# Optimization experiments

Measured on AMD Instinct MI355X. Metric: run time of the kernel, lower is better.

Reference implementation:

```python
import jax, jax.numpy as jnp
import numpy as np

EPS = 1e-5
D = 4  # max_displacement


def _conv(x, w, b, stride, pad):
    # x: [B,C,H,W], w: [O,I,kh,kw]
    y = jax.lax.conv_general_dilated(x, w, (stride, stride), [(pad, pad), (pad, pad)],
                                     dimension_numbers=('NCHW', 'OIHW', 'NCHW'))
    return y + b[None, :, None, None]


def _bn(x, g, b, m, v):
    # eval-mode batchnorm with running stats
    scale = (g * jax.lax.rsqrt(v + EPS))[None, :, None, None]
    return (x - m[None, :, None, None]) * scale + b[None, :, None, None]


def _extract(x, w1, b1, g1, be1, m1, v1, w2, b2, g2, be2, m2, v2, w3, b3, g3, be3, m3, v3):
    x = jax.nn.relu(_bn(_conv(x, w1, b1, 2, 3), g1, be1, m1, v1))
    x = jax.nn.relu(_bn(_conv(x, w2, b2, 2, 1), g2, be2, m2, v2))
    x = jax.nn.relu(_bn(_conv(x, w3, b3, 2, 1), g3, be3, m3, v3))
    return x  # [B,256,H/8,W/8]


def _correlation(x1, x2):
    # shifted-window correlation, 81 shifts (structural loop, static slices)
    B, C, H, W = x1.shape
    x2p = jnp.pad(x2, ((0, 0), (0, 0), (D, D), (D, D)))
    maps = [jnp.sum(x1 * x2p[:, :, i:i + H, j:j + W], axis=1)
            for i in range(2 * D + 1) for j in range(2 * D + 1)]
    return jnp.stack(maps, axis=1)  # [B,81,H,W]


def _gmm(cloth_img, person_img, fe, fw1, fb1, fw2, fb2, fw3, fb3):
    cf = _extract(cloth_img, *fe)
    pf = _extract(person_img, *fe)
    corr = _correlation(cf, pf)
    x = jax.nn.relu(_conv(corr, fw1, fb1, 1, 1))
    x = jax.nn.relu(_conv(x, fw2, fb2, 1, 1))
    return _conv(x, fw3, fb3, 1, 1)  # [B,2,H/8,W/8]


def setup_inputs() -> dict:
    key = jax.random.key(0)
    ks = jax.random.split(key, 32)
    B, H, W = 8, 512, 512
    w = lambda k, shape, s=0.05: jax.random.normal(k, shape, jnp.float32) * s
    inp = {}
    inp['cloth_img'] = jax.random.normal(ks[0], (B, 3, H, W), jnp.float32)
    inp['person_img'] = jax.random.normal(ks[1], (B, 3, H, W), jnp.float32)
    inp['w1'] = w(ks[2], (64, 3, 7, 7)); inp['b1'] = w(ks[3], (64,))
    inp['g1'] = 1.0 + w(ks[4], (64,)); inp['be1'] = w(ks[5], (64,))
    inp['m1'] = w(ks[6], (64,)); inp['v1'] = jax.random.uniform(ks[7], (64,), jnp.float32, 0.5, 1.5)
    inp['w2'] = w(ks[8], (128, 64, 3, 3)); inp['b2'] = w(ks[9], (128,))
    inp['g2'] = 1.0 + w(ks[10], (128,)); inp['be2'] = w(ks[11], (128,))
    inp['m2'] = w(ks[12], (128,)); inp['v2'] = jax.random.uniform(ks[13], (128,), jnp.float32, 0.5, 1.5)
    inp['w3'] = w(ks[14], (256, 128, 3, 3)); inp['b3'] = w(ks[15], (256,))
    inp['g3'] = 1.0 + w(ks[16], (256,)); inp['be3'] = w(ks[17], (256,))
    inp['m3'] = w(ks[18], (256,)); inp['v3'] = jax.random.uniform(ks[19], (256,), jnp.float32, 0.5, 1.5)
    inp['fw1'] = w(ks[20], (128, 81, 3, 3)); inp['fb1'] = w(ks[21], (128,))
    inp['fw2'] = w(ks[22], (64, 128, 3, 3)); inp['fb2'] = w(ks[23], (64,))
    inp['fw3'] = w(ks[24], (2, 64, 3, 3)); inp['fb3'] = w(ks[25], (2,))
    return inp


def reference(cloth_img, person_img,
              w1, b1, g1, be1, m1, v1,
              w2, b2, g2, be2, m2, v2,
              w3, b3, g3, be3, m3, v3,
              fw1, fb1, fw2, fb2, fw3, fb3):
    fe = (w1, b1, g1, be1, m1, v1, w2, b2, g2, be2, m2, v2, w3, b3, g3, be3, m3, v3)
    return _gmm(cloth_img, person_img, fe, fw1, fb1, fw2, fb2, fw3, fb3)
```

## Files before the change

### kernel.cpp

```cpp
#include <hip/hip_runtime.h>

typedef __bf16 bf16x8_t __attribute__((ext_vector_type(8)));
typedef float f32x4 __attribute__((ext_vector_type(4)));
typedef unsigned short u16x8 __attribute__((ext_vector_type(8)));
typedef unsigned short u16x4 __attribute__((ext_vector_type(4)));

#define EPS 1e-5f

__device__ __forceinline__ unsigned short f2bf(float f) {
    unsigned u = __builtin_bit_cast(unsigned, f);
    u += 0x7fff + ((u >> 16) & 1);
    return (unsigned short)(u >> 16);
}

__device__ __forceinline__ void gload16(const unsigned short* g, unsigned short* l) {
    __builtin_amdgcn_global_load_lds(
        (const __attribute__((address_space(1))) unsigned int*)g,
        (__attribute__((address_space(3))) unsigned int*)l,
        16, 0, 0);
}

template <int N> __device__ __forceinline__ void s_waitcnt_vm() {
    if constexpr (N == 0)       asm volatile("s_waitcnt vmcnt(0)" ::: "memory");
    else if constexpr (N == 8)  asm volatile("s_waitcnt vmcnt(8)" ::: "memory");
    else if constexpr (N == 10) asm volatile("s_waitcnt vmcnt(10)" ::: "memory");
    else if constexpr (N == 12) asm volatile("s_waitcnt vmcnt(12)" ::: "memory");
    else static_assert(N == 0, "unsupported vmcnt");
}

__global__ void prep_affine_all(const float* __restrict__ b1, const float* __restrict__ g1,
                                const float* __restrict__ be1, const float* __restrict__ m1,
                                const float* __restrict__ v1,
                                const float* __restrict__ b2, const float* __restrict__ g2,
                                const float* __restrict__ be2, const float* __restrict__ m2,
                                const float* __restrict__ v2,
                                const float* __restrict__ b3, const float* __restrict__ g3,
                                const float* __restrict__ be3, const float* __restrict__ m3,
                                const float* __restrict__ v3,
                                const float* __restrict__ fb1, const float* __restrict__ fb2,
                                const float* __restrict__ fb3, float* __restrict__ aff) {
    int i = blockIdx.x * 256 + threadIdx.x;
    if (i < 64) {
        float s = g1[i] * rsqrtf(v1[i] + EPS);
        aff[i] = s; aff[64 + i] = (b1[i] - m1[i]) * s + be1[i];
    } else if (i < 192) {
        int c = i - 64; float s = g2[c] * rsqrtf(v2[c] + EPS);
        aff[128 + c] = s; aff[256 + c] = (b2[c] - m2[c]) * s + be2[c];
    } else if (i < 448) {
        int c = i - 192; float s = g3[c] * rsqrtf(v3[c] + EPS);
        aff[384 + c] = s; aff[640 + c] = (b3[c] - m3[c]) * s + be3[c];
    } else if (i < 576) {
        int c = i - 448; aff[896 + c] = 1.f; aff[1024 + c] = fb1[c];
    } else if (i < 640) {
        int c = i - 576; aff[1152 + c] = 1.f; aff[1216 + c] = fb2[c];
    } else if (i < 642) {
        int c = i - 640; aff[1280 + c] = 1.f; aff[1288 + c] = fb3[c];
    }
}

__device__ __forceinline__ void wconv3x3(const float* __restrict__ w, unsigned short* __restrict__ dst,
                                         int Cout, int Sp, int Kp, int CIN, int CINP, int idx) {
    if (idx >= Sp * Kp) return;
    int m = idx / Kp, k = idx - m * Kp;
    int tap = k / CINP, ic = k - tap * CINP;
    unsigned short v = 0;
    if (m < Cout && tap < 9 && ic < CIN) {
        int kh = tap / 3, kw = tap - kh * 3;
        v = f2bf(w[((m * CIN + ic) * 3 + kh) * 3 + kw]);
    }
    dst[idx] = v;
}

__global__ void conv_weights_all(const float* __restrict__ w1, const float* __restrict__ w2,
                                 const float* __restrict__ w3, const float* __restrict__ fw1,
                                 const float* __restrict__ fw2, const float* __restrict__ fw3,
                                 unsigned short* d1, unsigned short* d2, unsigned short* d3,
                                 unsigned short* d4, unsigned short* d5, unsigned short* d6) {
    int idx = blockIdx.x * 256 + threadIdx.x;
    switch (blockIdx.y) {
    case 0: {
        if (idx >= 64 * 256) return;
        int m = idx >> 8, k = idx & 255;
        int kh = k >> 5, r = k & 31, kw = r >> 2, ic = r & 3;
        unsigned short v = 0;
        if (kh < 7 && kw < 7 && ic < 3) v = f2bf(w1[((m * 3 + ic) * 7 + kh) * 7 + kw]);
        d1[idx] = v;
    } break;
    case 1: wconv3x3(w2, d2, 128, 128, 576, 64, 64, idx); break;
    case 2: wconv3x3(w3, d3, 256, 256, 1152, 128, 128, idx); break;
    case 3: wconv3x3(fw1, d4, 128, 128, 1152, 81, 128, idx); break;
    case 4: wconv3x3(fw2, d5, 64, 64, 1152, 128, 128, idx); break;
    case 5: wconv3x3(fw3, d6, 2, 64, 576, 64, 64, idx); break;
    }
}

__global__ void to_nhwc4(const float* __restrict__ cloth, const float* __restrict__ person,
                         unsigned short* __restrict__ dst) {
    int z = blockIdx.z;
    const float* src = (z < 8) ? cloth + (size_t)z * 786432
                               : person + (size_t)(z - 8) * 786432;
    int p = blockIdx.x * 256 + threadIdx.x;
    int row = p >> 9, col = p & 511;
    u16x4 o;
    o[0] = f2bf(src[p]);
    o[1] = f2bf(src[262144 + p]);
    o[2] = f2bf(src[524288 + p]);
    o[3] = 0;
    *(u16x4*)&dst[(size_t)z * 1073296 + ((size_t)(row + 3) * 518 + col + 3) * 4] = o;
}

__global__ void border_zero(unsigned short* __restrict__ buf, int Hp, int Wp, int C8,
                            int imgStrideElems, int nimg) {
    int idx = blockIdx.x * 256 + threadIdx.x;
    int nb = 2 * Wp + 2 * (Hp - 2);
    int per = nb * C8;
    if (idx >= per * nimg) return;
    int z = idx / per, q = idx - z * per;
    int p = q / C8, cc = q - p * C8;
    int row, col;
    if (p < Wp) { row = 0; col = p; }
    else if (p < 2 * Wp) { row = Hp - 1; col = p - Wp; }
    else { int e = p - 2 * Wp; row = 1 + (e >> 1); col = (e & 1) ? Wp - 1 : 0; }
    const u16x8 zv = {0, 0, 0, 0, 0, 0, 0, 0};
    *(u16x8*)&buf[(size_t)z * imgStrideElems + ((size_t)row * Wp + col) * (C8 * 8) + cc * 8] = zv;
}

template <int WR, int WS, int MODE, bool RELU, bool OUT_NCHW, int CIN, int NKT,
          int HIN, int WOS, int STRIDE, int OPAD>
__global__ __launch_bounds__(WR * WS * 64)
void gemm_conv(const unsigned short* __restrict__ X, const unsigned short* __restrict__ Wmk,
               const float* __restrict__ scale, const float* __restrict__ shift,
               void* __restrict__ Yv, int Cout, int xImgStride, int yImgStride) {
    constexpr int BR = WR * 64, BS = WS * 64, NT = WR * WS * 64;
    constexpr int SXC = BR * 8 / NT, SWC = BS * 8 / NT;
    constexpr int NLOAD = SXC + SWC;
    constexpr int KP = (MODE == 1) ? NKT * 64 : 256;
    constexpr int WP = HIN + ((MODE == 2) ? 6 : 2);
    constexpr int WOUT = 1 << WOS;
    constexpr int WOP = WOUT + 2 * OPAD;
    __shared__ __align__(16) unsigned short Xs[2][BR * 64];
    __shared__ __align__(16) unsigned short Ws[2][BS * 64];
    const int tid = threadIdx.x;
    const int lane = tid & 63, wid = tid >> 6;
    const int wr = wid % WR, wsx = wid / WR;
    int bx = blockIdx.x;
    { const int nx = gridDim.x; bx = (bx & 7) * (nx >> 3) + (bx >> 3); }
    const int r0 = bx * BR, s0 = blockIdx.y * BS;
    const int z = blockIdx.z;
    const int lr = lane & 15, lk = lane >> 4;
    const unsigned short* Ximg = X + (size_t)z * xImgStride;

    const unsigned short* xsrc[SXC];
    #pragma unroll
    for (int i = 0; i < SXC; ++i) {
        int c = i * NT + tid;
        int row = c >> 3, chs = (c & 7) ^ (row & 7);
        int r = r0 + row;
        int oh = r >> WOS, ow = r & (WOUT - 1);
        if (MODE == 1)
            xsrc[i] = Ximg + ((size_t)(oh * STRIDE) * WP + (size_t)(ow * STRIDE)) * CIN + chs * 8;
        else
            xsrc[i] = Ximg + ((size_t)(2 * oh + (chs >> 2)) * WP + 2 * ow + (chs & 3) * 2) * 4;
    }
    const unsigned short* wsrc[SWC];
    #pragma unroll
    for (int i = 0; i < SWC; ++i) {
        int c = i * NT + tid;
        int row = c >> 3, chs = (c & 7) ^ (row & 7);
        wsrc[i] = Wmk + (size_t)(s0 + row) * KP + chs * 8;
    }

    int arow[4], brow[4];
    #pragma unroll
    for (int mi = 0; mi < 4; ++mi) arow[mi] = (wr * 64 + mi * 16 + lr) * 64;
    #pragma unroll
    for (int si = 0; si < 4; ++si) brow[si] = (wsx * 64 + si * 16 + lr) * 64;

    const f32x4 fz = {0.f, 0.f, 0.f, 0.f};
    f32x4 acc[4][4];
    #pragma unroll
    for (int a = 0; a < 4; ++a)
        #pragma unroll
        for (int b = 0; b < 4; ++b) acc[a][b] = fz;

    auto stage = [&](int kt, int b) {
        size_t koff;
        if (MODE == 1) {
            const int tap = (kt * 64) / CIN;
            const int kh = tap / 3, kw = tap - (tap / 3) * 3;
            const int icb0 = (kt * 64) % CIN;
            koff = ((size_t)kh * WP + kw) * CIN + icb0;
        } else {
            koff = (size_t)kt * 2 * WP * 4;
        }
        #pragma unroll
        for (int i = 0; i < SXC; ++i) gload16(xsrc[i] + koff, &Xs[b][(i * NT + wid * 64) * 8]);
        #pragma unroll
        for (int i = 0; i < SWC; ++i) gload16(wsrc[i] + (size_t)kt * 64, &Ws[b][(i * NT + wid * 64) * 8]);
    };

    stage(0, 0);
    #pragma unroll
    for (int kt = 0; kt < NKT; ++kt) {
        const int cur = kt & 1;
        if (kt + 1 < NKT) {
            stage(kt + 1, cur ^ 1);
            s_waitcnt_vm<NLOAD>();
        } else {
            s_waitcnt_vm<0>();
        }
        __builtin_amdgcn_sched_barrier(0);
        __builtin_amdgcn_s_barrier();
        __builtin_amdgcn_sched_barrier(0);

        #pragma unroll
        for (int hf = 0; hf < 2; ++hf) {
            const int cA = (((hf * 4 + lk) ^ (lr & 7)) * 8);
            u16x8 af[4], bfr[4];
            #pragma unroll
            for (int mi = 0; mi < 4; ++mi) af[mi] = *(const u16x8*)&Xs[cur][arow[mi] + cA];
            #pragma unroll
            for (int si = 0; si < 4; ++si) bfr[si] = *(const u16x8*)&Ws[cur][brow[si] + cA];
            #pragma unroll
            for (int mi = 0; mi < 4; ++mi)
                #pragma unroll
                for (int si = 0; si < 4; ++si)
                    acc[mi][si] = __builtin_amdgcn_mfma_f32_16x16x32_bf16(
                        __builtin_bit_cast(bf16x8_t, af[mi]),
                        __builtin_bit_cast(bf16x8_t, bfr[si]), acc[mi][si], 0, 0, 0);
        }
        __builtin_amdgcn_sched_barrier(0);
        __builtin_amdgcn_s_barrier();
    }

    if (OUT_NCHW) {
        #pragma unroll
        for (int si = 0; si < 4; ++si) {
            int col = s0 + wsx * 64 + si * 16 + lr;
            bool cok = col < Cout;
            float sc = cok ? scale[col] : 0.f;
            float sh = cok ? shift[col] : 0.f;
            #pragma unroll
            for (int mi = 0; mi < 4; ++mi) {
                int rbase = r0 + wr * 64 + mi * 16 + lk * 4;
                #pragma unroll
                for (int j = 0; j < 4; ++j) {
                    float v = acc[mi][si][j] * sc + sh;
                    if (RELU) v = fmaxf(v, 0.f);
                    if (cok) ((float*)Yv)[(size_t)z * yImgStride + col * 4096 + rbase + j] = v;
                }
            }
        }
    } else {
        unsigned short* epi = (unsigned short*)Xs;
        #pragma unroll
        for (int si = 0; si < 4; ++si) {
            int col = wsx * 64 + si * 16 + lr;
            float sc = scale[s0 + col];
            float sh = shift[s0 + col];
            #pragma unroll
            for (int mi = 0; mi < 4; ++mi) {
                int rowl = wr * 64 + mi * 16 + lk * 4;
                #pragma unroll
                for (int j = 0; j < 4; ++j) {
                    float v = acc[mi][si][j] * sc + sh;
                    if (RELU) v = fmaxf(v, 0.f);
                    epi[(rowl + j) * BS + col] = f2bf(v);
                }
            }
        }
        __syncthreads();
        constexpr int NCH = BR * BS / 8 / NT;
        constexpr int CPR = BS / 8;
        #pragma unroll
        for (int i = 0; i < NCH; ++i) {
            int c = i * NT + tid;
            int row = c / CPR, colc = c - (c / CPR) * CPR;
            int r = r0 + row;
            int oh = r >> WOS, ow = r & (WOUT - 1);
            size_t off = ((size_t)(oh + OPAD) * WOP + ow + OPAD) * Cout + s0 + colc * 8;
            *(u16x8*)((unsigned short*)Yv + (size_t)z * yImgStride + off) =
                *(const u16x8*)&epi[row * BS + colc * 8];
        }
    }
}

__global__ __launch_bounds__(256)
void corr_mfma(const unsigned short* __restrict__ cf,
               const unsigned short* __restrict__ pf,
               unsigned short* __restrict__ out) {
    const int h = blockIdx.x;
    const int z = blockIdx.y;
    const int tid = threadIdx.x;
    const int lane = tid & 63, t = tid >> 6;
    const int lr = lane & 15, lk = lane >> 4;
    const unsigned short* cfi = cf + (size_t)z * 1048576;
    const unsigned short* pfi = pf + (size_t)z * 1048576;
    unsigned short* outp = out + (size_t)z * 557568;

    u16x8 a[8];
    {
        const unsigned short* ap = cfi + ((size_t)(h * 64 + t * 16 + lr)) * 256 + lk * 8;
        #pragma unroll
        for (int ks = 0; ks < 8; ++ks) a[ks] = *(const u16x8*)(ap + ks * 32);
    }

    const u16x8 zz = {0, 0, 0, 0, 0, 0, 0, 0};
    for (int di = -4; di <= 4; ++di) {
        const int h2 = h + di;
        const bool hok = (unsigned)h2 < 64u;
        #pragma unroll
        for (int ct = 0; ct < 2; ++ct) {
            const int wpg = t * 16 - 8 + ct * 16 + lr;
            u16x8 b[8];
            if (hok && (unsigned)wpg < 64u) {
                const unsigned short* bp = pfi + ((size_t)(h2 * 64 + wpg)) * 256 + lk * 8;
                #pragma unroll
                for (int ks = 0; ks < 8; ++ks) b[ks] = *(const u16x8*)(bp + ks * 32);
            } else {
                #pragma unroll
                for (int ks = 0; ks < 8; ++ks) b[ks] = zz;
            }
            f32x4 acc0 = {0.f, 0.f, 0.f, 0.f}, acc1 = {0.f, 0.f, 0.f, 0.f};
            #pragma unroll
            for (int ks = 0; ks < 8; ks += 2) {
                acc0 = __builtin_amdgcn_mfma_f32_16x16x32_bf16(
                    __builtin_bit_cast(bf16x8_t, a[ks]),
                    __builtin_bit_cast(bf16x8_t, b[ks]), acc0, 0, 0, 0);
                acc1 = __builtin_amdgcn_mfma_f32_16x16x32_bf16(
                    __builtin_bit_cast(bf16x8_t, a[ks + 1]),
                    __builtin_bit_cast(bf16x8_t, b[ks + 1]), acc1, 0, 0, 0);
            }
            const int wl = lk * 4;
            const int wpl = ct * 16 - 8 + lr;
            #pragma unroll
            for (int j = 0; j < 4; ++j) {
                int dj = wpl - (wl + j);
                if (dj >= -4 && dj <= 4) {
                    int s = (di + 4) * 9 + dj + 4;
                    int w = t * 16 + wl + j;
                    outp[((size_t)(h + 1) * 66 + w + 1) * 128 + s] =
                        f2bf(acc0[j] + acc1[j]);
                }
            }
        }
    }
}

extern "C" void kernel_launch(void* const* d_in, const int* in_sizes, int n_in,
                              void* d_out, int out_size, void* d_ws, size_t ws_size,
                              hipStream_t stream) {
    const float* cloth  = (const float*)d_in[0];
    const float* person = (const float*)d_in[1];
    const float* w1 = (const float*)d_in[2];  const float* b1 = (const float*)d_in[3];
    const float* g1 = (const float*)d_in[4];  const float* be1 = (const float*)d_in[5];
    const float* m1 = (const float*)d_in[6];  const float* v1 = (const float*)d_in[7];
    const float* w2 = (const float*)d_in[8];  const float* b2 = (const float*)d_in[9];
    const float* g2 = (const float*)d_in[10]; const float* be2 = (const float*)d_in[11];
    const float* m2 = (const float*)d_in[12]; const float* v2 = (const float*)d_in[13];
    const float* w3 = (const float*)d_in[14]; const float* b3 = (const float*)d_in[15];
    const float* g3 = (const float*)d_in[16]; const float* be3 = (const float*)d_in[17];
    const float* m3 = (const float*)d_in[18]; const float* v3 = (const float*)d_in[19];
    const float* fw1 = (const float*)d_in[20]; const float* fb1 = (const float*)d_in[21];
    const float* fw2 = (const float*)d_in[22]; const float* fb2 = (const float*)d_in[23];
    const float* fw3 = (const float*)d_in[24]; const float* fb3 = (const float*)d_in[25];

    char* ws = (char*)d_ws;
    auto U = [&](size_t off) { return (unsigned short*)(ws + off); };
    unsigned short* nhwc = U(0);
    unsigned short* t1   = U(34345472);
    unsigned short* cf   = U(34345472);
    unsigned short* t2   = U(170668544);
    unsigned short* w1mk  = U(239890944);
    unsigned short* w2mk  = U(239923712);
    unsigned short* w3mk  = U(240071168);
    unsigned short* fw1mk = U(240660992);
    unsigned short* fw2mk = U(240955904);
    unsigned short* fw3mk = U(241103360);
    float* aff = (float*)(ws + 241177088);
    unsigned short* corr = U(241185280);
    unsigned short* f1b  = U(250106368);
    unsigned short* f2b  = U(259027456);
    float *s1 = aff,         *sh1 = aff + 64,   *s2 = aff + 128,  *sh2 = aff + 256;
    float *s3 = aff + 384,   *sh3 = aff + 640,  *sf1 = aff + 896, *shf1 = aff + 1024;
    float *sf2 = aff + 1152, *shf2 = aff + 1216, *sf3 = aff + 1280, *shf3 = aff + 1288;

    prep_affine_all<<<3, 256, 0, stream>>>(b1, g1, be1, m1, v1, b2, g2, be2, m2, v2,
                                           b3, g3, be3, m3, v3, fb1, fb2, fb3, aff);
    conv_weights_all<<<dim3(1152, 6), 256, 0, stream>>>(w1, w2, w3, fw1, fw2, fw3,
                                                        w1mk, w2mk, w3mk, fw1mk, fw2mk, fw3mk);

    hipMemsetAsync(ws, 0, 34345472, stream);
    hipMemsetAsync(ws + 241185280, 0, 22302720, stream);
    border_zero<<<514, 256, 0, stream>>>(t1, 258, 258, 8, 4260096, 16);
    border_zero<<<517, 256, 0, stream>>>(t2, 130, 130, 16, 2163200, 16);

    to_nhwc4<<<dim3(1024, 1, 16), 256, 0, stream>>>(cloth, person, nhwc);

    gemm_conv<4, 1, 2, true, false, 4, 4, 512, 8, 2, 1><<<dim3(256, 1, 16), 256, 0, stream>>>(
        nhwc, w1mk, s1, sh1, t1, 64, 1073296, 4260096);
    gemm_conv<2, 2, 1, true, false, 64, 9, 256, 7, 2, 1><<<dim3(128, 1, 16), 256, 0, stream>>>(
        t1, w2mk, s2, sh2, t2, 128, 4260096, 2163200);
    gemm_conv<2, 2, 1, true, false, 128, 18, 128, 6, 2, 0><<<dim3(32, 2, 16), 256, 0, stream>>>(
        t2, w3mk, s3, sh3, cf, 256, 2163200, 1048576);

    corr_mfma<<<dim3(64, 8), 256, 0, stream>>>(cf, cf + (size_t)8 * 1048576, corr);

    gemm_conv<2, 2, 1, true, false, 128, 18, 64, 6, 1, 1><<<dim3(32, 1, 8), 256, 0, stream>>>(
        corr, fw1mk, sf1, shf1, f1b, 128, 557568, 557568);
    gemm_conv<2, 1, 1, true, false, 128, 18, 64, 6, 1, 1><<<dim3(32, 1, 8), 128, 0, stream>>>(
        f1b, fw2mk, sf2, shf2, f2b, 64, 557568, 278784);
    gemm_conv<2, 1, 1, false, true, 64, 9, 64, 6, 1, 0><<<dim3(32, 1, 8), 128, 0, stream>>>(
        f2b, fw3mk, sf3, shf3, (float*)d_out, 2, 278784, 8192);
}
```

Measured before the change: 306.1 us.

## Add single-buffer conv path, padded epilogue LDS, and ring-only zeroing of input pad

Adds a PIPE template flag so the first conv (4-tap K loop) runs single-buffered with plain syncs and half the LDS, which should raise occupancy. The epilogue staging buffer gets a padded row stride to cut LDS bank conflicts, and shared memory becomes one buffer sized for the larger of GEMM and epilogue use. The large memset of the padded NHWC input is replaced by a kernel that zeroes only the 3-pixel border ring. The single-buffer path gives up load/compute overlap in that layer.

Result: faster. 271.2 us (-11.4%).

```diff
diff --git a/kernel.cpp b/kernel.cpp
--- a/kernel.cpp
+++ b/kernel.cpp
@@ -109,6 +109,18 @@
     *(u16x4*)&dst[(size_t)z * 1073296 + ((size_t)(row + 3) * 518 + col + 3) * 4] = o;
 }
 
+__global__ void ring3_zero(unsigned short* __restrict__ buf) {
+    int z = blockIdx.y;
+    int p = blockIdx.x * 256 + threadIdx.x;
+    if (p >= 6180) return;
+    int r, c;
+    if (p < 1554) { r = p / 518; c = p - (p / 518) * 518; }
+    else if (p < 3108) { int q = p - 1554; r = 515 + q / 518; c = q - (q / 518) * 518; }
+    else { int q = p - 3108; r = 3 + q / 6; int k = q - (q / 6) * 6; c = (k < 3) ? k : 512 + k; }
+    const u16x4 zv = {0, 0, 0, 0};
+    *(u16x4*)&buf[(size_t)z * 1073296 + ((size_t)r * 518 + c) * 4] = zv;
+}
+
 __global__ void border_zero(unsigned short* __restrict__ buf, int Hp, int Wp, int C8,
                             int imgStrideElems, int nimg) {
     int idx = blockIdx.x * 256 + threadIdx.x;
@@ -126,7 +138,7 @@
 }
 
 template <int WR, int WS, int MODE, bool RELU, bool OUT_NCHW, int CIN, int NKT,
-          int HIN, int WOS, int STRIDE, int OPAD>
+          int HIN, int WOS, int STRIDE, int OPAD, int PIPE>
 __global__ __launch_bounds__(WR * WS * 64)
 void gemm_conv(const unsigned short* __restrict__ X, const unsigned short* __restrict__ Wmk,
                const float* __restrict__ scale, const float* __restrict__ shift,
@@ -138,8 +150,14 @@
     constexpr int WP = HIN + ((MODE == 2) ? 6 : 2);
     constexpr int WOUT = 1 << WOS;
     constexpr int WOP = WOUT + 2 * OPAD;
-    __shared__ __align__(16) unsigned short Xs[2][BR * 64];
-    __shared__ __align__(16) unsigned short Ws[2][BS * 64];
+    constexpr int NBUF = PIPE ? 2 : 1;
+    constexpr int EPS_LDK = BS + 8;
+    constexpr int GEMM_ELEMS = NBUF * (BR + BS) * 64;
+    constexpr int EPI_ELEMS = BR * EPS_LDK;
+    constexpr int LDS_ELEMS = GEMM_ELEMS > EPI_ELEMS ? GEMM_ELEMS : EPI_ELEMS;
+    __shared__ __align__(16) unsigned short lds[LDS_ELEMS];
+    unsigned short* XsB = lds;
+    unsigned short* WsB = lds + NBUF * BR * 64;
     const int tid = threadIdx.x;
     const int lane = tid & 63, wid = tid >> 6;
     const int wr = wid % WR, wsx = wid / WR;
@@ -194,33 +212,21 @@
             koff = (size_t)kt * 2 * WP * 4;
         }
         #pragma unroll
-        for (int i = 0; i < SXC; ++i) gload16(xsrc[i] + koff, &Xs[b][(i * NT + wid * 64) * 8]);
-        #pragma unroll
-        for (int i = 0; i < SWC; ++i) gload16(wsrc[i] + (size_t)kt * 64, &Ws[b][(i * NT + wid * 64) * 8]);
+        for (int i = 0; i < SXC; ++i)
+            gload16(xsrc[i] + koff, &XsB[b * BR * 64 + (i * NT + wid * 64) * 8]);
+        #pragma unroll
+        for (int i = 0; i < SWC; ++i)
+            gload16(wsrc[i] + (size_t)kt * 64, &WsB[b * BS * 64 + (i * NT + wid * 64) * 8]);
     };
-
-    stage(0, 0);
-    #pragma unroll
-    for (int kt = 0; kt < NKT; ++kt) {
-        const int cur = kt & 1;
-        if (kt + 1 < NKT) {
-            stage(kt + 1, cur ^ 1);
-            s_waitcnt_vm<NLOAD>();
-        } else {
-            s_waitcnt_vm<0>();
-        }
-        __builtin_amdgcn_sched_barrier(0);
-        __builtin_amdgcn_s_barrier();
-        __builtin_amdgcn_sched_barrier(0);
-
+    auto compute = [&](int b) {
         #pragma unroll
         for (int hf = 0; hf < 2; ++hf) {
             const int cA = (((hf * 4 + lk) ^ (lr & 7)) * 8);
             u16x8 af[4], bfr[4];
             #pragma unroll
-            for (int mi = 0; mi < 4; ++mi) af[mi] = *(const u16x8*)&Xs[cur][arow[mi] + cA];
-            #pragma unroll
-            for (int si = 0; si < 4; ++si) bfr[si] = *(const u16x8*)&Ws[cur][brow[si] + cA];
+            for (int mi = 0; mi < 4; ++mi) af[mi] = *(const u16x8*)&XsB[b * BR * 64 + arow[mi] + cA];
+            #pragma unroll
+            for (int si = 0; si < 4; ++si) bfr[si] = *(const u16x8*)&WsB[b * BS * 64 + brow[si] + cA];
             #pragma unroll
             for (int mi = 0; mi < 4; ++mi)
                 #pragma unroll
@@ -229,8 +235,34 @@
                         __builtin_bit_cast(bf16x8_t, af[mi]),
                         __builtin_bit_cast(bf16x8_t, bfr[si]), acc[mi][si], 0, 0, 0);
         }
-        __builtin_amdgcn_sched_barrier(0);
-        __builtin_amdgcn_s_barrier();
+    };
+
+    if (PIPE == 0) {
+        #pragma unroll
+        for (int kt = 0; kt < NKT; ++kt) {
+            stage(kt, 0);
+            __syncthreads();
+            compute(0);
+            __syncthreads();
+        }
+    } else {
+        stage(0, 0);
+        #pragma unroll
+        for (int kt = 0; kt < NKT; ++kt) {
+            const int cur = kt & 1;
+            if (kt + 1 < NKT) {
+                stage(kt + 1, cur ^ 1);
+                s_waitcnt_vm<NLOAD>();
+            } else {
+                s_waitcnt_vm<0>();
+            }
+            __builtin_amdgcn_sched_barrier(0);
+            __builtin_amdgcn_s_barrier();
+            __builtin_amdgcn_sched_barrier(0);
+            compute(cur);
+            __builtin_amdgcn_sched_barrier(0);
+            __builtin_amdgcn_s_barrier();
+        }
     }
 
     if (OUT_NCHW) {
@@ -252,7 +284,8 @@
             }
         }
     } else {
-        unsigned short* epi = (unsigned short*)Xs;
+        __syncthreads();
+        unsigned short* epi = lds;
         #pragma unroll
         for (int si = 0; si < 4; ++si) {
             int col = wsx * 64 + si * 16 + lr;
@@ -265,7 +298,7 @@
                 for (int j = 0; j < 4; ++j) {
                     float v = acc[mi][si][j] * sc + sh;
                     if (RELU) v = fmaxf(v, 0.f);
-                    epi[(rowl + j) * BS + col] = f2bf(v);
+                    epi[(rowl + j) * EPS_LDK + col] = f2bf(v);
                 }
             }
         }
@@ -280,7 +313,7 @@
             int oh = r >> WOS, ow = r & (WOUT - 1);
             size_t off = ((size_t)(oh + OPAD) * WOP + ow + OPAD) * Cout + s0 + colc * 8;
             *(u16x8*)((unsigned short*)Yv + (size_t)z * yImgStride + off) =
-                *(const u16x8*)&epi[row * BS + colc * 8];
+                *(const u16x8*)&epi[row * EPS_LDK + colc * 8];
         }
     }
 }
@@ -390,26 +423,26 @@
     conv_weights_all<<<dim3(1152, 6), 256, 0, stream>>>(w1, w2, w3, fw1, fw2, fw3,
                                                         w1mk, w2mk, w3mk, fw1mk, fw2mk, fw3mk);
 
-    hipMemsetAsync(ws, 0, 34345472, stream);
+    ring3_zero<<<dim3(25, 16), 256, 0, stream>>>(nhwc);
     hipMemsetAsync(ws + 241185280, 0, 22302720, stream);
     border_zero<<<514, 256, 0, stream>>>(t1, 258, 258, 8, 4260096, 16);
     border_zero<<<517, 256, 0, stream>>>(t2, 130, 130, 16, 2163200, 16);
 
     to_nhwc4<<<dim3(1024, 1, 16), 256, 0, stream>>>(cloth, person, nhwc);
 
-    gemm_conv<4, 1, 2, true, false, 4, 4, 512, 8, 2, 1><<<dim3(256, 1, 16), 256, 0, stream>>>(
+    gemm_conv<4, 1, 2, true, false, 4, 4, 512, 8, 2, 1, 0><<<dim3(256, 1, 16), 256, 0, stream>>>(
         nhwc, w1mk, s1, sh1, t1, 64, 1073296, 4260096);
-    gemm_conv<2, 2, 1, true, false, 64, 9, 256, 7, 2, 1><<<dim3(128, 1, 16), 256, 0, stream>>>(
+    gemm_conv<2, 2, 1, true, false, 64, 9, 256, 7, 2, 1, 1><<<dim3(128, 1, 16), 256, 0, stream>>>(
         t1, w2mk, s2, sh2, t2, 128, 4260096, 2163200);
-    gemm_conv<2, 2, 1, true, false, 128, 18, 128, 6, 2, 0><<<dim3(32, 2, 16), 256, 0, stream>>>(
+    gemm_conv<2, 2, 1, true, false, 128, 18, 128, 6, 2, 0, 1><<<dim3(32, 2, 16), 256, 0, stream>>>(
         t2, w3mk, s3, sh3, cf, 256, 2163200, 1048576);
 
     corr_mfma<<<dim3(64, 8), 256, 0, stream>>>(cf, cf + (size_t)8 * 1048576, corr);
 
-    gemm_conv<2, 2, 1, true, false, 128, 18, 64, 6, 1, 1><<<dim3(32, 1, 8), 256, 0, stream>>>(
+    gemm_conv<2, 2, 1, true, false, 128, 18, 64, 6, 1, 1, 1><<<dim3(32, 1, 8), 256, 0, stream>>>(
         corr, fw1mk, sf1, shf1, f1b, 128, 557568, 557568);
-    gemm_conv<2, 1, 1, true, false, 128, 18, 64, 6, 1, 1><<<dim3(32, 1, 8), 128, 0, stream>>>(
+    gemm_conv<2, 1, 1, true, false, 128, 18, 64, 6, 1, 1, 1><<<dim3(32, 1, 8), 128, 0, stream>>>(
         f1b, fw2mk, sf2, shf2, f2b, 64, 557568, 278784);
-    gemm_conv<2, 1, 1, false, true, 64, 9, 64, 6, 1, 0><<<dim3(32, 1, 8), 128, 0, stream>>>(
+    gemm_conv<2, 1, 1, false, true, 64, 9, 64, 6, 1, 0, 1><<<dim3(32, 1, 8), 128, 0, stream>>>(
         f2b, fw3mk, sf3, shf3, (float*)d_out, 2, 278784, 8192);
 }
```
